# Performance work log

Measured on AMD Instinct MI355X. Metric: run time of the kernel, lower is better.

Reference implementation:

```python
import jax, jax.numpy as jnp
import numpy as np

B, C, H, W = 32, 384, 56, 56
SPARSE = 8
HEADS = 8
HIDDEN = 4 * C
EPS = 1e-5


def _ln(x, g, b):
    m = jnp.mean(x, axis=-1, keepdims=True)
    v = jnp.mean((x - m) ** 2, axis=-1, keepdims=True)
    return (x - m) * jax.lax.rsqrt(v + EPS) * g + b


def setup_inputs() -> dict:
    key = jax.random.key(0)
    ks = jax.random.split(key, 12)
    s = 0.02
    return {
        "x": jax.random.normal(ks[0], (B, C, H, W), jnp.float32),
        "ln1_g": jnp.ones((C,), jnp.float32),
        "ln1_b": jnp.zeros((C,), jnp.float32),
        "qkv_w": jax.random.normal(ks[1], (C, 3 * C), jnp.float32) * s,
        "proj_w": jax.random.normal(ks[2], (C, C), jnp.float32) * s,
        "proj_b": jnp.zeros((C,), jnp.float32),
        "ln2_g": jnp.ones((C,), jnp.float32),
        "ln2_b": jnp.zeros((C,), jnp.float32),
        "fc1_w": jax.random.normal(ks[3], (C, HIDDEN), jnp.float32) * s,
        "fc1_b": jnp.zeros((HIDDEN,), jnp.float32),
        "dw_w": jax.random.normal(ks[4], (HIDDEN, 1, 3, 3), jnp.float32) * np.sqrt(2.0 / 9.0),
        "dw_b": jnp.zeros((HIDDEN,), jnp.float32),
        "fc2_w": jax.random.normal(ks[5], (HIDDEN, C), jnp.float32) * s,
        "fc2_b": jnp.zeros((C,), jnp.float32),
        "gamma1": jnp.full((C,), 1e-6, jnp.float32),
        "gamma2": jnp.full((C,), 1e-6, jnp.float32),
    }


def reference(x, ln1_g, ln1_b, qkv_w, proj_w, proj_b, ln2_g, ln2_b,
              fc1_w, fc1_b, dw_w, dw_b, fc2_w, fc2_b, gamma1, gamma2):
    Bx, Cx, Hx, Wx = x.shape
    s = SPARSE
    g = Hx // s  # grid size; H divisible by sparse_size per module assert
    N = Hx * Wx
    hd = Cx // HEADS
    scale = hd ** (-0.5)

    x_before = x.reshape(Bx, Cx, N).transpose(0, 2, 1)  # [B,N,C]

    # alter_sparse: gather tokens spaced g apart into s x s windows
    xw = x.transpose(0, 2, 3, 1).reshape(Bx, s, g, s, g, Cx)
    xw = xw.transpose(0, 2, 4, 1, 3, 5).reshape(Bx * g * g, s * s, Cx)

    # attention on windows
    h = _ln(xw, ln1_g, ln1_b)
    qkv = (h @ qkv_w).reshape(Bx * g * g, s * s, 3, HEADS, hd)
    q, k, v = (qkv[:, :, i].transpose(0, 2, 1, 3) for i in range(3))  # [Bw,h,n,d]
    attn = jax.nn.softmax(jnp.einsum('bhqd,bhkd->bhqk', q, k) * scale, axis=-1)
    o = jnp.einsum('bhqk,bhkd->bhqd', attn, v).transpose(0, 2, 1, 3)
    o = o.reshape(Bx * g * g, s * s, Cx) @ proj_w + proj_b

    # alter_unsparse: scatter windows back to spatial layout
    o = o.reshape(Bx, g, g, s, s, Cx).transpose(0, 3, 1, 4, 2, 5)
    o = o.reshape(Bx, Hx, Wx, Cx).reshape(Bx, N, Cx)

    x1 = x_before + gamma1 * o

    # MLP with depthwise conv
    m = _ln(x1, ln2_g, ln2_b) @ fc1_w + fc1_b  # [B,N,hidden]
    m2 = m.transpose(0, 2, 1).reshape(Bx, HIDDEN, Hx, Wx)
    m2 = jax.lax.conv_general_dilated(
        m2, dw_w, window_strides=(1, 1), padding=((1, 1), (1, 1)),
        dimension_numbers=('NCHW', 'OIHW', 'NCHW'),
        feature_group_count=HIDDEN) + dw_b[None, :, None, None]
    m = m2.reshape(Bx, HIDDEN, N).transpose(0, 2, 1)
    m = jax.nn.gelu(m, approximate=False)
    m = m @ fc2_w + fc2_b

    x2 = x1 + gamma2 * m
    return x2.transpose(0, 2, 1).reshape(Bx, Cx, Hx, Wx)
```

## Files before the change

### kernel.cpp

```cpp
#include <hip/hip_runtime.h>
#include <hip/hip_bf16.h>

typedef __hip_bfloat16 bf16;
typedef float v4f __attribute__((ext_vector_type(4)));
typedef __attribute__((ext_vector_type(8))) short short8;

__device__ __forceinline__ float b2f(bf16 v) { return __bfloat162float(v); }
__device__ __forceinline__ bf16 f2b(float v) { return __float2bfloat16(v); }

__device__ __forceinline__ void gload_lds16(const bf16* g, bf16* l) {
    __builtin_amdgcn_global_load_lds((__attribute__((address_space(1))) void*)(void*)g,
                                     (__attribute__((address_space(3))) void*)l, 16, 0, 0);
}

#define BB 32
#define CD 384
#define HH 56
#define ND 3136
#define HID 1536
#define GG 7
#define SS 8
#define MROWS 100352

__device__ __forceinline__ int wrow_to_token(int orow) {
    int w = orow >> 6, t = orow & 63;
    int bb = w / 49, wr = w % 49;
    int gy = wr / GG, gx = wr % GG;
    int sy = t >> 3, sx = t & 7;
    return bb * ND + (sy * GG + gy) * HH + (sx * GG + gx);
}

__global__ __launch_bounds__(256) void transpose_f2b_k(const float* __restrict__ in,
                                                       bf16* __restrict__ out, int R, int Cc)
{
    __shared__ float tile[32][33];
    int c0 = blockIdx.x * 32, r0 = blockIdx.y * 32;
    size_t bb = blockIdx.z;
    int tx = threadIdx.x & 31, ty = threadIdx.x >> 5;
    const float* ip = in + bb * (size_t)R * Cc;
    bf16* op = out + bb * (size_t)R * Cc;
#pragma unroll
    for (int i = 0; i < 4; i++)
        tile[ty + i * 8][tx] = ip[(size_t)(r0 + ty + i * 8) * Cc + (c0 + tx)];
    __syncthreads();
#pragma unroll
    for (int i = 0; i < 4; i++)
        op[(size_t)(c0 + ty + i * 8) * R + (r0 + tx)] = f2b(tile[tx][ty + i * 8]);
}

__global__ __launch_bounds__(256) void ln_k(const bf16* __restrict__ in,
                                            const float* __restrict__ g,
                                            const float* __restrict__ b,
                                            bf16* __restrict__ out,
                                            int row0, int gather)
{
    int wave = threadIdx.x >> 6, lane = threadIdx.x & 63;
    int row = row0 + blockIdx.x * 4 + wave;
    int src = gather ? wrow_to_token(row) : row;
    const bf16* ip = in + (size_t)src * CD;
    float vals[6];
    float s = 0.f, s2 = 0.f;
#pragma unroll
    for (int i = 0; i < 6; i++) {
        float v = b2f(ip[lane + i * 64]);
        vals[i] = v; s += v; s2 += v * v;
    }
#pragma unroll
    for (int off = 32; off >= 1; off >>= 1) {
        s  += __shfl_xor(s, off);
        s2 += __shfl_xor(s2, off);
    }
    float mean = s * (1.f / CD);
    float var = s2 * (1.f / CD) - mean * mean;
    float rstd = rsqrtf(var + 1e-5f);
    bf16* op = out + (size_t)(row - row0) * CD;
#pragma unroll
    for (int i = 0; i < 6; i++) {
        int c = lane + i * 64;
        op[c] = f2b((vals[i] - mean) * rstd * g[c] + b[c]);
    }
}

__global__ __launch_bounds__(256) void gemm_bt(const bf16* __restrict__ A,
                                               const bf16* __restrict__ Bt,
                                               const float* __restrict__ bias,
                                               bf16* __restrict__ Cm,
                                               int M, int N, int K, int gx,
                                               const bf16* __restrict__ xt,
                                               const float* __restrict__ g1,
                                               int row0)
{
    __shared__ __align__(16) bf16 As[2][128][32];
    __shared__ __align__(16) bf16 Bs[2][128][32];
    const int nwg = gridDim.x;
    const int q = nwg >> 3, r = nwg & 7;
    const int xcd = blockIdx.x & 7, id8 = blockIdx.x >> 3;
    const int wgid = (xcd < r ? xcd * (q + 1) : r * (q + 1) + (xcd - r) * q) + id8;
    const int m0 = (wgid / gx) * 128, n0 = (wgid % gx) * 128;

    const int tid = threadIdx.x;
    const int lane = tid & 63, wave = tid >> 6;
    const int rb = (wave >> 1) * 64, cb = (wave & 1) * 64;
    const int lr = lane & 15, ko = (lane >> 4) * 8;
    const int r0s = wave * 32;
    const int srow = lane >> 2;
    const int scol = (lane & 3) * 8;

    auto STAGE = [&](int bi, int kk0) {
#pragma unroll
        for (int h = 0; h < 2; h++) {
            int row = r0s + h * 16 + srow;
            gload_lds16(&A [(size_t)(m0 + row) * K + kk0 + scol], &As[bi][r0s + h * 16][0]);
            gload_lds16(&Bt[(size_t)(n0 + row) * K + kk0 + scol], &Bs[bi][r0s + h * 16][0]);
        }
    };

    v4f acc[4][4];
#pragma unroll
    for (int i = 0; i < 4; i++)
#pragma unroll
        for (int j = 0; j < 4; j++) acc[i][j] = (v4f)0.f;

    const int nt = K >> 5;
    int cur = 0;
    STAGE(0, 0);

    for (int t = 0; t < nt; t++) {
        if (t + 1 < nt) {
            STAGE(cur ^ 1, (t + 1) << 5);
            asm volatile("s_waitcnt vmcnt(4)" ::: "memory");
        } else {
            asm volatile("s_waitcnt vmcnt(0)" ::: "memory");
        }
        __builtin_amdgcn_s_barrier();
        __builtin_amdgcn_sched_barrier(0);

        short8 af[4], bfr[4];
#pragma unroll
        for (int mi = 0; mi < 4; mi++) af[mi]  = *(const short8*)&As[cur][rb + mi * 16 + lr][ko];
#pragma unroll
        for (int ni = 0; ni < 4; ni++) bfr[ni] = *(const short8*)&Bs[cur][cb + ni * 16 + lr][ko];
#pragma unroll
        for (int mi = 0; mi < 4; mi++)
#pragma unroll
            for (int ni = 0; ni < 4; ni++)
                acc[mi][ni] = __builtin_amdgcn_mfma_f32_16x16x32_bf16(af[mi], bfr[ni], acc[mi][ni], 0, 0, 0);

        asm volatile("s_waitcnt lgkmcnt(0)" ::: "memory");
        __builtin_amdgcn_sched_barrier(0);
        __builtin_amdgcn_s_barrier();
        cur ^= 1;
    }

#pragma unroll
    for (int ni = 0; ni < 4; ni++) {
        int col = n0 + cb + ni * 16 + lr;
        float bv = bias ? bias[col] : 0.f;
#pragma unroll
        for (int mi = 0; mi < 4; mi++) {
            int rowb = m0 + rb + mi * 16 + (lane >> 4) * 4;
            if (g1 == nullptr) {
#pragma unroll
                for (int r2 = 0; r2 < 4; r2++)
                    Cm[(size_t)(rowb + r2) * N + col] = f2b(acc[mi][ni][r2] + bv);
            } else {
                float gv = g1[col];
#pragma unroll
                for (int r2 = 0; r2 < 4; r2++) {
                    int token = wrow_to_token(row0 + rowb + r2);
                    size_t xi = (size_t)token * CD + col;
                    Cm[xi] = f2b(b2f(xt[xi]) + gv * (acc[mi][ni][r2] + bv));
                }
            }
        }
    }
}

__global__ __launch_bounds__(64) void attn_mfma_k(const bf16* __restrict__ qkv,
                                                  bf16* __restrict__ o)
{
    __shared__ __align__(16) char lds[14336];
    char* Ps = lds;
    bf16* Vs = (bf16*)(lds + 8192);

    const int lane = threadIdx.x;
    const int lr = lane & 15, grp = lane >> 4;
    const int lw = blockIdx.x >> 3, head = blockIdx.x & 7;

    const bf16* base = qkv + (size_t)lw * 64 * 1152 + head * 48;

#pragma unroll
    for (int it = 0; it < 6; it++) {
        int i = it * 64 + lane;
        int t = i / 6, s = i - t * 6;
        *(uint4*)((char*)Vs + t * 96 + s * 16) =
            *(const uint4*)(base + (size_t)t * 1152 + 768 + s * 8);
    }

    v4f accs[4][4];
#pragma unroll
    for (int mi = 0; mi < 4; mi++)
#pragma unroll
        for (int ni = 0; ni < 4; ni++) accs[mi][ni] = (v4f)0.f;

    const short8 z8 = (short8)0;
    {
        short8 qf[4], kf[4];
#pragma unroll
        for (int mi = 0; mi < 4; mi++)
            qf[mi] = *(const short8*)(base + (size_t)(mi * 16 + lr) * 1152 + grp * 8);
#pragma unroll
        for (int ni = 0; ni < 4; ni++)
            kf[ni] = *(const short8*)(base + 384 + (size_t)(ni * 16 + lr) * 1152 + grp * 8);
#pragma unroll
        for (int mi = 0; mi < 4; mi++)
#pragma unroll
            for (int ni = 0; ni < 4; ni++)
                accs[mi][ni] = __builtin_amdgcn_mfma_f32_16x16x32_bf16(qf[mi], kf[ni], accs[mi][ni], 0, 0, 0);
#pragma unroll
        for (int mi = 0; mi < 4; mi++)
            qf[mi] = (grp < 2) ? *(const short8*)(base + (size_t)(mi * 16 + lr) * 1152 + 32 + grp * 8) : z8;
#pragma unroll
        for (int ni = 0; ni < 4; ni++)
            kf[ni] = (grp < 2) ? *(const short8*)(base + 384 + (size_t)(ni * 16 + lr) * 1152 + 32 + grp * 8) : z8;
#pragma unroll
        for (int mi = 0; mi < 4; mi++)
#pragma unroll
            for (int ni = 0; ni < 4; ni++)
                accs[mi][ni] = __builtin_amdgcn_mfma_f32_16x16x32_bf16(qf[mi], kf[ni], accs[mi][ni], 0, 0, 0);
    }

    const float scale = 0.14433756729740643f;
#pragma unroll
    for (int mi = 0; mi < 4; mi++)
#pragma unroll
        for (int ni = 0; ni < 4; ni++) accs[mi][ni] *= scale;

    float inv_s[4][4];
#pragma unroll
    for (int mi = 0; mi < 4; mi++) {
#pragma unroll
        for (int r = 0; r < 4; r++) {
            float mx = fmaxf(fmaxf(accs[mi][0][r], accs[mi][1][r]),
                             fmaxf(accs[mi][2][r], accs[mi][3][r]));
#pragma unroll
            for (int off = 8; off >= 1; off >>= 1) mx = fmaxf(mx, __shfl_xor(mx, off));
            float sum = 0.f;
#pragma unroll
            for (int ni = 0; ni < 4; ni++) {
                float e = __expf(accs[mi][ni][r] - mx);
                accs[mi][ni][r] = e;
                sum += e;
            }
#pragma unroll
            for (int off = 8; off >= 1; off >>= 1) sum += __shfl_xor(sum, off);
            inv_s[mi][r] = 1.f / sum;
        }
    }

#pragma unroll
    for (int mi = 0; mi < 4; mi++)
#pragma unroll
        for (int ni = 0; ni < 4; ni++)
#pragma unroll
            for (int r = 0; r < 4; r++) {
                int i = mi * 16 + grp * 4 + r;
                int j = ni * 16 + lr;
                int byte = (i * 128 + j * 2) ^ ((i & 7) << 4);
                *(bf16*)(Ps + byte) = f2b(accs[mi][ni][r]);
            }

    v4f acco[4][3];
#pragma unroll
    for (int mi = 0; mi < 4; mi++)
#pragma unroll
        for (int ni = 0; ni < 3; ni++) acco[mi][ni] = (v4f)0.f;

    const short* vsp = (const short*)Vs;
#pragma unroll
    for (int kk = 0; kk < 2; kk++) {
        int k0 = kk * 32 + grp * 8;
        short8 pf[4];
#pragma unroll
        for (int mi = 0; mi < 4; mi++) {
            int row = mi * 16 + lr;
            int byte = (row * 128 + k0 * 2) ^ ((row & 7) << 4);
            pf[mi] = *(const short8*)(Ps + byte);
        }
        short8 vf[3];
#pragma unroll
        for (int ni = 0; ni < 3; ni++) {
#pragma unroll
            for (int jj = 0; jj < 8; jj++)
                vf[ni][jj] = vsp[(k0 + jj) * 48 + ni * 16 + lr];
        }
#pragma unroll
        for (int mi = 0; mi < 4; mi++)
#pragma unroll
            for (int ni = 0; ni < 3; ni++)
                acco[mi][ni] = __builtin_amdgcn_mfma_f32_16x16x32_bf16(pf[mi], vf[ni], acco[mi][ni], 0, 0, 0);
    }

    bf16* op = o + (size_t)lw * 64 * CD + head * 48;
#pragma unroll
    for (int mi = 0; mi < 4; mi++)
#pragma unroll
        for (int r = 0; r < 4; r++) {
            int t = mi * 16 + grp * 4 + r;
            float is = inv_s[mi][r];
#pragma unroll
            for (int ni = 0; ni < 3; ni++)
                op[(size_t)t * CD + ni * 16 + lr] = f2b(acco[mi][ni][r] * is);
        }
}

__global__ __launch_bounds__(256) void dwconv_gelu_k(const bf16* __restrict__ m1c,
                                                     const float* __restrict__ wgt,
                                                     const float* __restrict__ bias,
                                                     bf16* __restrict__ gc)
{
    const int c  = blockIdx.x * 64 + (threadIdx.x & 63);
    const int xq = threadIdx.x >> 6;
    const int xx = blockIdx.y * 8 + xq * 2;
    const int lb = blockIdx.z >> 2;
    const int ys = (blockIdx.z & 3) * 14;

    float w9[9];
#pragma unroll
    for (int i = 0; i < 9; i++) w9[i] = wgt[c * 9 + i];
    const float bs = bias[c];

    const bf16* base = m1c + (size_t)lb * ND * HID + c;
    bool  v[4];
    const bf16* colp[4];
#pragma unroll
    for (int i = 0; i < 4; i++) {
        int xc = xx - 1 + i;
        v[i] = (xc >= 0 && xc < HH);
        int xcl = xc < 0 ? 0 : (xc > HH - 1 ? HH - 1 : xc);
        colp[i] = base + (size_t)xcl * HID;
    }
    const size_t ystride = (size_t)HH * HID;

    float win[3][4];
    {
        int ym = ys - 1;
        int ymc = ym < 0 ? 0 : ym;
        bool yv = (ym >= 0);
#pragma unroll
        for (int i = 0; i < 4; i++)
            win[0][i] = (yv && v[i]) ? b2f(colp[i][(size_t)ymc * ystride]) : 0.f;
#pragma unroll
        for (int i = 0; i < 4; i++)
            win[1][i] = v[i] ? b2f(colp[i][(size_t)ys * ystride]) : 0.f;
    }

#pragma unroll
    for (int s = 0; s < 14; s++) {
        const int y = ys + s;
        const int yp = y + 1;
        const bool yv = (yp < HH);
        const int ypc = yv ? yp : (HH - 1);
#pragma unroll
        for (int i = 0; i < 4; i++)
            win[2][i] = (yv && v[i]) ? b2f(colp[i][(size_t)ypc * ystride]) : 0.f;

        float a0 = bs, a1 = bs;
#pragma unroll
        for (int r = 0; r < 3; r++)
#pragma unroll
            for (int j = 0; j < 3; j++) {
                a0 = fmaf(w9[r * 3 + j], win[r][j],     a0);
                a1 = fmaf(w9[r * 3 + j], win[r][j + 1], a1);
            }
        float g0 = 0.5f * a0 * (1.f + erff(a0 * 0.70710678118654752f));
        float g1 = 0.5f * a1 * (1.f + erff(a1 * 0.70710678118654752f));
        size_t o0 = ((size_t)lb * ND + (size_t)y * HH + xx) * HID + c;
        gc[o0]       = f2b(g0);
        gc[o0 + HID] = f2b(g1);

#pragma unroll
        for (int i = 0; i < 4; i++) { win[0][i] = win[1][i]; win[1][i] = win[2][i]; }
    }
}

__global__ __launch_bounds__(256) void resid2_k(const bf16* __restrict__ x1,
                                                const bf16* __restrict__ m2c,
                                                const float* __restrict__ gamma2,
                                                float* __restrict__ out, int b0)
{
    __shared__ float tile[32][33];
    int n0 = blockIdx.x * 32, c0 = blockIdx.y * 32;
    int lb = blockIdx.z, gb = b0 + lb;
    int tx = threadIdx.x & 31, ty = threadIdx.x >> 5;
#pragma unroll
    for (int i = 0; i < 4; i++) {
        int n = n0 + ty + i * 8, c = c0 + tx;
        size_t sx1 = ((size_t)gb * ND + n) * CD + c;
        size_t sm  = ((size_t)lb * ND + n) * CD + c;
        tile[ty + i * 8][tx] = b2f(x1[sx1]) + gamma2[c] * b2f(m2c[sm]);
    }
    __syncthreads();
#pragma unroll
    for (int i = 0; i < 4; i++) {
        int c = c0 + ty + i * 8, n = n0 + tx;
        out[((size_t)gb * CD + c) * ND + n] = tile[tx][ty + i * 8];
    }
}

extern "C" void kernel_launch(void* const* d_in, const int* in_sizes, int n_in,
                              void* d_out, int out_size, void* d_ws, size_t ws_size,
                              hipStream_t stream) {
    const float* x      = (const float*)d_in[0];
    const float* ln1_g  = (const float*)d_in[1];
    const float* ln1_b  = (const float*)d_in[2];
    const float* qkv_w  = (const float*)d_in[3];
    const float* proj_w = (const float*)d_in[4];
    const float* proj_b = (const float*)d_in[5];
    const float* ln2_g  = (const float*)d_in[6];
    const float* ln2_b  = (const float*)d_in[7];
    const float* fc1_w  = (const float*)d_in[8];
    const float* fc1_b  = (const float*)d_in[9];
    const float* dw_w   = (const float*)d_in[10];
    const float* dw_b   = (const float*)d_in[11];
    const float* fc2_w  = (const float*)d_in[12];
    const float* fc2_b  = (const float*)d_in[13];
    const float* gamma1 = (const float*)d_in[14];
    const float* gamma2 = (const float*)d_in[15];
    float* out = (float*)d_out;

    const size_t SZ_TOK = (size_t)MROWS * CD * 2;
    const size_t S0 = 2 * SZ_TOK;
    const size_t WTS = 3538944;

    const size_t attn_end8 = S0 + (size_t)(MROWS / 8) * CD * 2 + (size_t)(MROWS / 8) * 1152 * 2;
    int cm = 16;
    {
        size_t mc2 = (size_t)(BB / 8) * ND;
        size_t mlp_end8 = S0 + mc2 * CD * 2 + 2 * mc2 * HID * 2;
        size_t tot8 = (mlp_end8 > attn_end8 ? mlp_end8 : attn_end8) + WTS;
        if (ws_size >= tot8) cm = 8;
    }
    const int nb = BB / cm;
    const int Mc2 = nb * ND;
    const size_t sz_h2 = (size_t)Mc2 * CD * 2;
    const size_t sz_m1 = (size_t)Mc2 * HID * 2;
    const size_t mlp_end = S0 + sz_h2 + 2 * sz_m1;

    int ca = 0;
    size_t sz_h = 0, sz_qk = 0, attn_end = 0;
    for (int cand = 2; cand <= 8 && !ca; cand <<= 1) {
        int McA_ = MROWS / cand;
        size_t h_ = (size_t)McA_ * CD * 2, qk_ = (size_t)McA_ * 1152 * 2;
        size_t ae = S0 + h_ + qk_;
        size_t tot = (mlp_end > ae ? mlp_end : ae) + WTS;
        if (ws_size >= tot) { ca = cand; sz_h = h_; sz_qk = qk_; attn_end = ae; }
    }
    if (!ca) return;
    const int McA = MROWS / ca;

    const size_t Wo = (mlp_end > attn_end ? mlp_end : attn_end);

    char* w = (char*)d_ws;
    bf16* xt      = (bf16*)(w + 0);
    bf16* x1      = (bf16*)(w + SZ_TOK);
    bf16* hc      = (bf16*)(w + S0);
    bf16* qkvc    = (bf16*)(w + S0 + sz_h);
    bf16* h2c     = (bf16*)(w + S0);
    bf16* m1c     = (bf16*)(w + S0 + sz_h2);
    bf16* gc      = (bf16*)(w + S0 + sz_h2 + sz_m1);
    bf16* qkv_wt  = (bf16*)(w + Wo);
    bf16* proj_wt = (bf16*)(w + Wo + 884736);
    bf16* fc1_wt  = (bf16*)(w + Wo + 884736 + 294912);
    bf16* fc2_wt  = (bf16*)(w + Wo + 884736 + 294912 + 1179648);

    dim3 blk(256);

    transpose_f2b_k<<<dim3(98, 12, 32), blk, 0, stream>>>(x, xt, CD, ND);
    transpose_f2b_k<<<dim3(36, 12, 1), blk, 0, stream>>>(qkv_w, qkv_wt, CD, 1152);
    transpose_f2b_k<<<dim3(12, 12, 1), blk, 0, stream>>>(proj_w, proj_wt, CD, CD);
    transpose_f2b_k<<<dim3(48, 12, 1), blk, 0, stream>>>(fc1_w, fc1_wt, CD, HID);
    transpose_f2b_k<<<dim3(12, 48, 1), blk, 0, stream>>>(fc2_w, fc2_wt, HID, CD);

    for (int ch = 0; ch < ca; ch++) {
        int row0 = ch * McA;
        ln_k<<<McA / 4, blk, 0, stream>>>(xt, ln1_g, ln1_b, hc, row0, 1);
        gemm_bt<<<dim3(9 * (McA / 128)), blk, 0, stream>>>(hc, qkv_wt, nullptr, qkvc,
                                                           McA, 1152, CD, 9, nullptr, nullptr, 0);
        attn_mfma_k<<<(McA / 64) * 8, dim3(64), 0, stream>>>(qkvc, hc);
        gemm_bt<<<dim3(3 * (McA / 128)), blk, 0, stream>>>(hc, proj_wt, proj_b, x1,
                                                           McA, CD, CD, 3, xt, gamma1, row0);
    }

    for (int ch = 0; ch < cm; ch++) {
        int r0 = ch * Mc2, b0 = ch * nb;
        ln_k<<<Mc2 / 4, blk, 0, stream>>>(x1, ln2_g, ln2_b, h2c, r0, 0);
        gemm_bt<<<dim3(12 * (Mc2 / 128)), blk, 0, stream>>>(h2c, fc1_wt, fc1_b, m1c,
                                                            Mc2, HID, CD, 12, nullptr, nullptr, 0);
        dwconv_gelu_k<<<dim3(HID / 64, 7, nb * 4), blk, 0, stream>>>(m1c, dw_w, dw_b, gc);
        gemm_bt<<<dim3(3 * (Mc2 / 128)), blk, 0, stream>>>(gc, fc2_wt, fc2_b, h2c,
                                                           Mc2, CD, HID, 3, nullptr, nullptr, 0);
        resid2_k<<<dim3(98, 12, nb), blk, 0, stream>>>(x1, h2c, gamma2, out, b0);
    }
}
```

Measured before the change: 1.817 ms.

## Replace double-buffered GEMM staging with single buffer and widen MLP chunk search

The GEMM kernel drops its double-buffered LDS pipeline, where the next K-tile's loads overlapped the current tile's MFMAs. It now loads one tile, syncs, computes, and syncs again, which halves LDS use and may raise occupancy. The cost is exposed global-load latency on every K step. Separately, the host now searches chunk counts 2, 4 and 8 for the MLP and picks the smallest that fits the workspace, so fewer, larger MLP chunks can be launched.

```diff
diff --git a/kernel.cpp b/kernel.cpp
--- a/kernel.cpp
+++ b/kernel.cpp
@@ -90,8 +90,8 @@
                                                const float* __restrict__ g1,
                                                int row0)
 {
-    __shared__ __align__(16) bf16 As[2][128][32];
-    __shared__ __align__(16) bf16 Bs[2][128][32];
+    __shared__ __align__(16) bf16 As[128][32];
+    __shared__ __align__(16) bf16 Bs[128][32];
     const int nwg = gridDim.x;
     const int q = nwg >> 3, r = nwg & 7;
     const int xcd = blockIdx.x & 7, id8 = blockIdx.x >> 3;
@@ -106,50 +106,31 @@
     const int srow = lane >> 2;
     const int scol = (lane & 3) * 8;
 
-    auto STAGE = [&](int bi, int kk0) {
+    v4f acc[4][4];
+#pragma unroll
+    for (int i = 0; i < 4; i++)
+#pragma unroll
+        for (int j = 0; j < 4; j++) acc[i][j] = (v4f)0.f;
+
+    for (int kk = 0; kk < K; kk += 32) {
 #pragma unroll
         for (int h = 0; h < 2; h++) {
             int row = r0s + h * 16 + srow;
-            gload_lds16(&A [(size_t)(m0 + row) * K + kk0 + scol], &As[bi][r0s + h * 16][0]);
-            gload_lds16(&Bt[(size_t)(n0 + row) * K + kk0 + scol], &Bs[bi][r0s + h * 16][0]);
-        }
-    };
-
-    v4f acc[4][4];
-#pragma unroll
-    for (int i = 0; i < 4; i++)
-#pragma unroll
-        for (int j = 0; j < 4; j++) acc[i][j] = (v4f)0.f;
-
-    const int nt = K >> 5;
-    int cur = 0;
-    STAGE(0, 0);
-
-    for (int t = 0; t < nt; t++) {
-        if (t + 1 < nt) {
-            STAGE(cur ^ 1, (t + 1) << 5);
-            asm volatile("s_waitcnt vmcnt(4)" ::: "memory");
-        } else {
-            asm volatile("s_waitcnt vmcnt(0)" ::: "memory");
-        }
-        __builtin_amdgcn_s_barrier();
-        __builtin_amdgcn_sched_barrier(0);
-
+            gload_lds16(&A [(size_t)(m0 + row) * K + kk + scol], &As[r0s + h * 16][0]);
+            gload_lds16(&Bt[(size_t)(n0 + row) * K + kk + scol], &Bs[r0s + h * 16][0]);
+        }
+        __syncthreads();
         short8 af[4], bfr[4];
 #pragma unroll
-        for (int mi = 0; mi < 4; mi++) af[mi]  = *(const short8*)&As[cur][rb + mi * 16 + lr][ko];
-#pragma unroll
-        for (int ni = 0; ni < 4; ni++) bfr[ni] = *(const short8*)&Bs[cur][cb + ni * 16 + lr][ko];
+        for (int mi = 0; mi < 4; mi++) af[mi]  = *(const short8*)&As[rb + mi * 16 + lr][ko];
+#pragma unroll
+        for (int ni = 0; ni < 4; ni++) bfr[ni] = *(const short8*)&Bs[cb + ni * 16 + lr][ko];
 #pragma unroll
         for (int mi = 0; mi < 4; mi++)
 #pragma unroll
             for (int ni = 0; ni < 4; ni++)
                 acc[mi][ni] = __builtin_amdgcn_mfma_f32_16x16x32_bf16(af[mi], bfr[ni], acc[mi][ni], 0, 0, 0);
-
-        asm volatile("s_waitcnt lgkmcnt(0)" ::: "memory");
-        __builtin_amdgcn_sched_barrier(0);
-        __builtin_amdgcn_s_barrier();
-        cur ^= 1;
+        __syncthreads();
     }
 
 #pragma unroll
@@ -434,12 +415,13 @@
     const size_t WTS = 3538944;
 
     const size_t attn_end8 = S0 + (size_t)(MROWS / 8) * CD * 2 + (size_t)(MROWS / 8) * 1152 * 2;
+
     int cm = 16;
-    {
-        size_t mc2 = (size_t)(BB / 8) * ND;
-        size_t mlp_end8 = S0 + mc2 * CD * 2 + 2 * mc2 * HID * 2;
-        size_t tot8 = (mlp_end8 > attn_end8 ? mlp_end8 : attn_end8) + WTS;
-        if (ws_size >= tot8) cm = 8;
+    for (int cand = 2; cand < 16; cand <<= 1) {
+        size_t mc2 = (size_t)(BB / cand) * ND;
+        size_t me = S0 + mc2 * CD * 2 + 2 * mc2 * HID * 2;
+        size_t tot = (me > attn_end8 ? me : attn_end8) + WTS;
+        if (ws_size >= tot) { cm = cand; break; }
     }
     const int nb = BB / cm;
     const int Mc2 = nb * ND;
@@ -448,13 +430,13 @@
     const size_t mlp_end = S0 + sz_h2 + 2 * sz_m1;
 
     int ca = 0;
-    size_t sz_h = 0, sz_qk = 0, attn_end = 0;
+    size_t sz_h = 0, attn_end = 0;
     for (int cand = 2; cand <= 8 && !ca; cand <<= 1) {
         int McA_ = MROWS / cand;
         size_t h_ = (size_t)McA_ * CD * 2, qk_ = (size_t)McA_ * 1152 * 2;
         size_t ae = S0 + h_ + qk_;
         size_t tot = (mlp_end > ae ? mlp_end : ae) + WTS;
-        if (ws_size >= tot) { ca = cand; sz_h = h_; sz_qk = qk_; attn_end = ae; }
+        if (ws_size >= tot) { ca = cand; sz_h = h_; attn_end = ae; }
     }
     if (!ca) return;
     const int McA = MROWS / ca;
```

Measured after the change: 1.697 ms. 1.07x faster.
